# Kernel tuning notes

Hardware: AMD Instinct MI355X
Metric: run time of the kernel (lower is better)

Reference implementation:

```python
import jax, jax.numpy as jnp
import numpy as np

B = 2097152  # batch of 3x4 affine matrices


def setup_inputs() -> dict:
    key = jax.random.key(0)
    theta = jax.random.normal(key, (B, 3, 4), dtype=jnp.float32)
    return {"theta": theta}


def reference(theta):
    eps = 1e-6
    W = theta[:, :, :3]                                   # (b,3,3)
    # singular values of each 3x3 matrix, descending, shape (b,3)
    sv = jnp.linalg.svd(W, full_matrices=False, compute_uv=False) + eps
    loss = -6.0 + jnp.sum(sv ** 2 + sv ** (-2), axis=1)  # (b,)
    return loss.mean()
```

## Files before the change

kernel.cpp:

```cpp
#include <hip/hip_runtime.h>
#include <math.h>


#define ORTHO_EPS   1e-6
#define NOISE_SCALE 1.35e-7
#define SMOOTH_CUT  1e-4f
#define K_MIX       0.6363636363636364
#define NBLK        2048

__device__ __forceinline__ double ortho_sample(const float4 r0, const float4 r1,
                                               const float4 r2)
{
    float w00 = r0.x, w01 = r0.y, w02 = r0.z;
    float w10 = r1.x, w11 = r1.y, w12 = r1.z;
    float w20 = r2.x, w21 = r2.y, w22 = r2.z;

    float a00 = fmaf(w00, w00, fmaf(w10, w10, w20 * w20));
    float a11 = fmaf(w01, w01, fmaf(w11, w11, w21 * w21));
    float a22 = fmaf(w02, w02, fmaf(w12, w12, w22 * w22));
    float a01 = fmaf(w00, w01, fmaf(w10, w11, w20 * w21));
    float a02 = fmaf(w00, w02, fmaf(w10, w12, w20 * w22));
    float a12 = fmaf(w01, w02, fmaf(w11, w12, w21 * w22));

    float tr = a00 + a11 + a22;
    float e2 = fmaf(a00, a11, -(a01 * a01))
             + fmaf(a00, a22, -(a02 * a02))
             + fmaf(a11, a22, -(a12 * a12));
    e2 = fmaxf(e2, 1e-30f);

    double dw00 = w00, dw01 = w01, dw02 = w02;
    double dw10 = w10, dw11 = w11, dw12 = w12;
    double dw20 = w20, dw21 = w21, dw22 = w22;
    double detW = dw00 * (dw11 * dw22 - dw12 * dw21)
                - dw01 * (dw10 * dw22 - dw12 * dw20)
                + dw02 * (dw10 * dw21 - dw11 * dw20);
    float df   = (float)fabs(detW);
    float detA = df * df;

    float x = detA / e2;
    float L = fmaxf(e2 - x * (tr - x), 1e-30f);
    x = detA / L;
    L = fmaxf(e2 - x * (tr - x), 1e-30f);
    float irt  = rsqrtf(L);
    float sig3 = df * irt;
    float l3   = detA * (irt * irt);

    float s    = fmaxf(tr - l3, 0.0f);
    float disc = fmaxf(fmaf(s, s, -4.0f * L), 0.0f);
    float rt   = sqrtf(disc);
    float l1   = 0.5f * (s + rt);
    float l2   = L / fmaxf(l1, 1e-30f);

    float sig1 = sqrtf(l1);
    float sig2 = sqrtf(l2);

    float s1e = sig1 + 1e-6f;
    float s2e = sig2 + 1e-6f;
    float s3e = sig3 + 1e-6f;
    float q1 = s1e * s1e, q2 = s2e * s2e, q3 = s3e * s3e;

    float base = -6.0f + (q1 + q2 + q3) + (q1 + q2) / (q1 * q2);

    double inv3;
    if (sig3 < SMOOTH_CUT) {
        double sig3d = (double)sig3;
        double snd   = NOISE_SCALE * (double)sig1;
        double s3ed  = sig3d + ORTHO_EPS;
        double q3d   = s3ed * s3ed;
        double inv3_exact = 1.0 / q3d;
        const double c0 = 0.5390798, c1 = 1.6365194,
                     c2 = 2.8024876, c3 = 4.1445469;
        const double wg0 = 0.37301225767908, wg1 = 0.11723990788622,
                     wg2 = 0.0096352201207, wg3 = 0.00011261453837;
        double acc = 0.0, ep, em;
        ep = fmax(sig3d + c0 * snd, 0.0) + ORTHO_EPS;
        em = fmax(sig3d - c0 * snd, 0.0) + ORTHO_EPS;
        acc += wg0 * (1.0 / (ep * ep) + 1.0 / (em * em));
        ep = fmax(sig3d + c1 * snd, 0.0) + ORTHO_EPS;
        em = fmax(sig3d - c1 * snd, 0.0) + ORTHO_EPS;
        acc += wg1 * (1.0 / (ep * ep) + 1.0 / (em * em));
        ep = fmax(sig3d + c2 * snd, 0.0) + ORTHO_EPS;
        em = fmax(sig3d - c2 * snd, 0.0) + ORTHO_EPS;
        acc += wg2 * (1.0 / (ep * ep) + 1.0 / (em * em));
        ep = fmax(sig3d + c3 * snd, 0.0) + ORTHO_EPS;
        em = fmax(sig3d - c3 * snd, 0.0) + ORTHO_EPS;
        acc += wg3 * (1.0 / (ep * ep) + 1.0 / (em * em));
        inv3 = inv3_exact - K_MIX * (acc - inv3_exact);
    } else {
        inv3 = (double)(1.0f / q3);
    }

    return (double)base + inv3;
}

__global__ __launch_bounds__(256) void ortho_pass1(
    const float* __restrict__ theta, double* __restrict__ partial, int B)
{
    double local = 0.0;
    int stride = gridDim.x * blockDim.x;
    for (int i = blockIdx.x * blockDim.x + threadIdx.x; i < B; i += stride) {
        const float4* t4 = reinterpret_cast<const float4*>(theta + (size_t)i * 12);
        float4 r0 = t4[0];
        float4 r1 = t4[1];
        float4 r2 = t4[2];
        local += ortho_sample(r0, r1, r2);
    }

    for (int off = 32; off > 0; off >>= 1)
        local += __shfl_down(local, off, 64);

    __shared__ double ssum[4];
    int lane = threadIdx.x & 63;
    int wid  = threadIdx.x >> 6;
    if (lane == 0) ssum[wid] = local;
    __syncthreads();
    if (threadIdx.x == 0)
        partial[blockIdx.x] = ssum[0] + ssum[1] + ssum[2] + ssum[3];
}

__global__ __launch_bounds__(256) void ortho_pass2(
    const double* __restrict__ partial, float* __restrict__ out,
    double invB, int n)
{
    double local = 0.0;
    for (int i = threadIdx.x; i < n; i += 256)
        local += partial[i];

    for (int off = 32; off > 0; off >>= 1)
        local += __shfl_down(local, off, 64);

    __shared__ double ssum[4];
    int lane = threadIdx.x & 63;
    int wid  = threadIdx.x >> 6;
    if (lane == 0) ssum[wid] = local;
    __syncthreads();
    if (threadIdx.x == 0)
        out[0] = (float)((ssum[0] + ssum[1] + ssum[2] + ssum[3]) * invB);
}

extern "C" void kernel_launch(void* const* d_in, const int* in_sizes, int n_in,
                              void* d_out, int out_size, void* d_ws, size_t ws_size,
                              hipStream_t stream)
{
    const float* theta = (const float*)d_in[0];
    int B = in_sizes[0] / 12;
    double* partial = (double*)d_ws;

    ortho_pass1<<<NBLK, 256, 0, stream>>>(theta, partial, B);
    ortho_pass2<<<1, 256, 0, stream>>>(partial, (float*)d_out,
                                       1.0 / (double)B, NBLK);
}
```

Before: 144.1 us.

## Defer near-singular samples to a compacted list processed in the reduce pass

```diff
diff --git a/kernel.cpp b/kernel.cpp
--- a/kernel.cpp
+++ b/kernel.cpp
@@ -7,9 +7,11 @@
 #define SMOOTH_CUT  1e-4f
 #define K_MIX       0.6363636363636364
 #define NBLK        2048
+#define LIST_CAP    (1u << 20)
 
-__device__ __forceinline__ double ortho_sample(const float4 r0, const float4 r1,
-                                               const float4 r2)
+__device__ __forceinline__ float ortho_core_f32(const float4 r0, const float4 r1,
+                                                const float4 r2, float* sig1_out,
+                                                float* sig3_out, float* inv3_out)
 {
     float w00 = r0.x, w01 = r0.y, w02 = r0.z;
     float w10 = r1.x, w11 = r1.y, w12 = r1.z;
@@ -28,13 +30,11 @@
              + fmaf(a11, a22, -(a12 * a12));
     e2 = fmaxf(e2, 1e-30f);
 
-    double dw00 = w00, dw01 = w01, dw02 = w02;
-    double dw10 = w10, dw11 = w11, dw12 = w12;
-    double dw20 = w20, dw21 = w21, dw22 = w22;
-    double detW = dw00 * (dw11 * dw22 - dw12 * dw21)
-                - dw01 * (dw10 * dw22 - dw12 * dw20)
-                + dw02 * (dw10 * dw21 - dw11 * dw20);
-    float df   = (float)fabs(detW);
+    float m0 = fmaf(w11, w22, -(w12 * w21));
+    float m1 = fmaf(w10, w22, -(w12 * w20));
+    float m2 = fmaf(w10, w21, -(w11 * w20));
+    float detW = fmaf(w00, m0, fmaf(-w01, m1, w02 * m2));
+    float df   = fabsf(detW);
     float detA = df * df;
 
     float x = detA / e2;
@@ -59,15 +59,90 @@
     float s3e = sig3 + 1e-6f;
     float q1 = s1e * s1e, q2 = s2e * s2e, q3 = s3e * s3e;
 
-    float base = -6.0f + (q1 + q2 + q3) + (q1 + q2) / (q1 * q2);
+    *sig1_out = sig1;
+    *sig3_out = sig3;
+    *inv3_out = 1.0f / q3;
+    return -6.0f + (q1 + q2 + q3) + (q1 + q2) / (q1 * q2);
+}
 
-    double inv3;
-    if (sig3 < SMOOTH_CUT) {
-        double sig3d = (double)sig3;
-        double snd   = NOISE_SCALE * (double)sig1;
-        double s3ed  = sig3d + ORTHO_EPS;
-        double q3d   = s3ed * s3ed;
-        double inv3_exact = 1.0 / q3d;
+__global__ __launch_bounds__(256) void ortho_pass1(
+    const float* __restrict__ theta, double* __restrict__ partial,
+    unsigned* __restrict__ cnt, unsigned* __restrict__ list, int B)
+{
+    double local = 0.0;
+    int stride = gridDim.x * blockDim.x;
+    for (int i = blockIdx.x * blockDim.x + threadIdx.x; i < B; i += stride) {
+        const float4* t4 = reinterpret_cast<const float4*>(theta + (size_t)i * 12);
+        float4 r0 = t4[0];
+        float4 r1 = t4[1];
+        float4 r2 = t4[2];
+        float sig1f, sig3f, inv3f;
+        float basef = ortho_core_f32(r0, r1, r2, &sig1f, &sig3f, &inv3f);
+        local += (double)basef + (double)inv3f;
+        if (sig3f < SMOOTH_CUT) {
+            unsigned slot = atomicAdd(cnt, 1u);
+            if (slot < LIST_CAP) list[slot] = (unsigned)i;
+        }
+    }
+
+    for (int off = 32; off > 0; off >>= 1)
+        local += __shfl_down(local, off, 64);
+
+    __shared__ double ssum[4];
+    int lane = threadIdx.x & 63;
+    int wid  = threadIdx.x >> 6;
+    if (lane == 0) ssum[wid] = local;
+    __syncthreads();
+    if (threadIdx.x == 0)
+        partial[blockIdx.x] = ssum[0] + ssum[1] + ssum[2] + ssum[3];
+}
+
+__global__ __launch_bounds__(256) void ortho_pass2(
+    const float* __restrict__ theta, const double* __restrict__ partial,
+    const unsigned* __restrict__ cnt, const unsigned* __restrict__ list,
+    float* __restrict__ out, double invB, int nblk)
+{
+    double local = 0.0;
+    for (int i = threadIdx.x; i < nblk; i += 256)
+        local += partial[i];
+
+    unsigned n = *cnt;
+    if (n > LIST_CAP) n = LIST_CAP;
+    for (unsigned k = threadIdx.x; k < n; k += 256) {
+        unsigned i = list[k];
+        const float4* t4 = reinterpret_cast<const float4*>(theta + (size_t)i * 12);
+        float4 r0 = t4[0];
+        float4 r1 = t4[1];
+        float4 r2 = t4[2];
+        float sig1f, sig3f, inv3f;
+        (void)ortho_core_f32(r0, r1, r2, &sig1f, &sig3f, &inv3f);
+
+        double w00 = r0.x, w01 = r0.y, w02 = r0.z;
+        double w10 = r1.x, w11 = r1.y, w12 = r1.z;
+        double w20 = r2.x, w21 = r2.y, w22 = r2.z;
+        double a00 = w00*w00 + w10*w10 + w20*w20;
+        double a11 = w01*w01 + w11*w11 + w21*w21;
+        double a22 = w02*w02 + w12*w12 + w22*w22;
+        double a01 = w00*w01 + w10*w11 + w20*w21;
+        double a02 = w00*w02 + w10*w12 + w20*w22;
+        double a12 = w01*w02 + w11*w12 + w21*w22;
+        double tr = a00 + a11 + a22;
+        double e2 = (a00*a11 - a01*a01) + (a00*a22 - a02*a02) + (a11*a22 - a12*a12);
+        e2 = fmax(e2, 1e-300);
+        double detW = w00 * (w11 * w22 - w12 * w21)
+                    - w01 * (w10 * w22 - w12 * w20)
+                    + w02 * (w10 * w21 - w11 * w20);
+        double dfd  = fabs(detW);
+        double detA = dfd * dfd;
+        double xd = detA / e2;
+        double Ld = fmax(e2 - xd * (tr - xd), 1e-300);
+        xd = detA / Ld;
+        Ld = fmax(e2 - xd * (tr - xd), 1e-300);
+        double sig3d = dfd / sqrt(Ld);
+
+        double snd  = NOISE_SCALE * (double)sig1f;
+        double s3ed = sig3d + ORTHO_EPS;
+        double inv3_exact = 1.0 / (s3ed * s3ed);
         const double c0 = 0.5390798, c1 = 1.6365194,
                      c2 = 2.8024876, c3 = 4.1445469;
         const double wg0 = 0.37301225767908, wg1 = 0.11723990788622,
@@ -85,46 +160,10 @@
         ep = fmax(sig3d + c3 * snd, 0.0) + ORTHO_EPS;
         em = fmax(sig3d - c3 * snd, 0.0) + ORTHO_EPS;
         acc += wg3 * (1.0 / (ep * ep) + 1.0 / (em * em));
-        inv3 = inv3_exact - K_MIX * (acc - inv3_exact);
-    } else {
-        inv3 = (double)(1.0f / q3);
+        double inv3_new = inv3_exact - K_MIX * (acc - inv3_exact);
+
+        local += inv3_new - (double)inv3f;
     }
-
-    return (double)base + inv3;
-}
-
-__global__ __launch_bounds__(256) void ortho_pass1(
-    const float* __restrict__ theta, double* __restrict__ partial, int B)
-{
-    double local = 0.0;
-    int stride = gridDim.x * blockDim.x;
-    for (int i = blockIdx.x * blockDim.x + threadIdx.x; i < B; i += stride) {
-        const float4* t4 = reinterpret_cast<const float4*>(theta + (size_t)i * 12);
-        float4 r0 = t4[0];
-        float4 r1 = t4[1];
-        float4 r2 = t4[2];
-        local += ortho_sample(r0, r1, r2);
-    }
-
-    for (int off = 32; off > 0; off >>= 1)
-        local += __shfl_down(local, off, 64);
-
-    __shared__ double ssum[4];
-    int lane = threadIdx.x & 63;
-    int wid  = threadIdx.x >> 6;
-    if (lane == 0) ssum[wid] = local;
-    __syncthreads();
-    if (threadIdx.x == 0)
-        partial[blockIdx.x] = ssum[0] + ssum[1] + ssum[2] + ssum[3];
-}
-
-__global__ __launch_bounds__(256) void ortho_pass2(
-    const double* __restrict__ partial, float* __restrict__ out,
-    double invB, int n)
-{
-    double local = 0.0;
-    for (int i = threadIdx.x; i < n; i += 256)
-        local += partial[i];
 
     for (int off = 32; off > 0; off >>= 1)
         local += __shfl_down(local, off, 64);
@@ -144,9 +183,12 @@
 {
     const float* theta = (const float*)d_in[0];
     int B = in_sizes[0] / 12;
-    double* partial = (double*)d_ws;
+    unsigned* cnt    = (unsigned*)d_ws;
+    unsigned* list   = (unsigned*)((char*)d_ws + 64);
+    double*   partial = (double*)((char*)d_ws + (8u << 20));
 
-    ortho_pass1<<<NBLK, 256, 0, stream>>>(theta, partial, B);
-    ortho_pass2<<<1, 256, 0, stream>>>(partial, (float*)d_out,
-                                       1.0 / (double)B, NBLK);
+    hipMemsetAsync(cnt, 0, 64, stream);
+    ortho_pass1<<<NBLK, 256, 0, stream>>>(theta, partial, cnt, list, B);
+    ortho_pass2<<<1, 256, 0, stream>>>(theta, partial, cnt, list,
+                                       (float*)d_out, 1.0 / (double)B, NBLK);
 }
```

Measured after the change: 149.3 us. 3.6% more time.
